# Kernel optimization log

Measured on AMD Instinct MI355X. Metric: run time of the kernel, lower is better.

Reference implementation:

```python
import jax, jax.numpy as jnp
import numpy as np

D_MODEL = 1024
NUM_HEADS = 16
HEAD_DIM = D_MODEL // NUM_HEADS


def setup_inputs() -> dict:
    key = jax.random.key(0)
    ks = jax.random.split(key, 10)
    s = 1.0 / np.sqrt(D_MODEL)
    return {
        "x": jax.random.normal(ks[0], (2, 2048, D_MODEL), dtype=jnp.float32),
        "Wq": jax.random.normal(ks[1], (D_MODEL, D_MODEL), dtype=jnp.float32) * s,
        "bq": jnp.zeros((D_MODEL,), jnp.float32),
        "Wk": jax.random.normal(ks[2], (D_MODEL, D_MODEL), dtype=jnp.float32) * s,
        "bk": jnp.zeros((D_MODEL,), jnp.float32),
        "Wv": jax.random.normal(ks[3], (D_MODEL, D_MODEL), dtype=jnp.float32) * s,
        "bv": jnp.zeros((D_MODEL,), jnp.float32),
        "Wo": jax.random.normal(ks[4], (D_MODEL, D_MODEL), dtype=jnp.float32) * s,
        "bo": jnp.zeros((D_MODEL,), jnp.float32),
        "rotary": jax.random.normal(ks[5], (1, 1, HEAD_DIM), dtype=jnp.float32) * 0.02,
    }


def reference(x, Wq, bq, Wk, bk, Wv, bv, Wo, bo, rotary):
    B, S, _ = x.shape
    H, Dh = NUM_HEADS, HEAD_DIM
    q = (x @ Wq + bq).reshape(B, S, H, Dh)
    k = (x @ Wk + bk).reshape(B, S, H, Dh)
    v = (x @ Wv + bv).reshape(B, S, H, Dh)
    # additive learned bias broadcast over (B, S, H) -> rotary has shape (1,1,Dh)
    q_rot = q + rotary[:, :, None, :]  # (B,S,H,Dh)
    scale = 1.0 / jnp.sqrt(jnp.asarray(Dh, jnp.float32))
    attn = jnp.einsum('bqhd,bkhd->bhqk', q_rot, k) * scale
    attn = jax.nn.softmax(attn, axis=-1)  # dropout is identity in eval / p=0
    out = jnp.einsum('bhqk,bkhd->bqhd', attn, v).reshape(B, S, H * Dh)
    return out @ Wo + bo
```

## Files before the change

### kernel.cpp

```cpp
#include <hip/hip_runtime.h>
#include <hip/hip_bf16.h>
#include <hip/hip_fp16.h>
#include <cstdint>

typedef _Float16 f16;
typedef _Float16 f16x4 __attribute__((ext_vector_type(4)));
typedef _Float16 f16x8 __attribute__((ext_vector_type(8)));
typedef __fp16 h16x2 __attribute__((ext_vector_type(2)));
typedef float f32x4 __attribute__((ext_vector_type(4)));

constexpr int D_MODEL = 1024;
constexpr int NH = 16;
constexpr int DH = 64;
constexpr int BATCH = 2;
constexpr int SEQ = 2048;
constexpr int NTOK = BATCH * SEQ;

static __device__ __forceinline__ void gld_lds16(const void* g, void* l) {
  __builtin_amdgcn_global_load_lds(
      (__attribute__((address_space(1))) void*)(g),
      (__attribute__((address_space(3))) void*)(l), 16, 0, 0);
}

static __device__ __forceinline__ f16x4 pack4(float a, float b, float c, float d) {
  h16x2 lo = __builtin_amdgcn_cvt_pkrtz(a, b);
  h16x2 hi = __builtin_amdgcn_cvt_pkrtz(c, d);
  struct { h16x2 x, y; } pr{lo, hi};
  return __builtin_bit_cast(f16x4, pr);
}


__global__ void cvt_x(const float* __restrict__ x, f16* __restrict__ xh) {
  int i = blockIdx.x * blockDim.x + threadIdx.x;
  const float4* p = reinterpret_cast<const float4*>(x) + (size_t)i * 2;
  float4 a = p[0], b = p[1];
  f16x8 o;
  o[0] = (f16)a.x; o[1] = (f16)a.y; o[2] = (f16)a.z; o[3] = (f16)a.w;
  o[4] = (f16)b.x; o[5] = (f16)b.y; o[6] = (f16)b.z; o[7] = (f16)b.w;
  *reinterpret_cast<f16x8*>(xh + (size_t)i * 8) = o;
}

__global__ void cvt_w(const float* __restrict__ Wq, const float* __restrict__ Wk,
                      const float* __restrict__ Wv, const float* __restrict__ Wo,
                      f16* __restrict__ Wqkvt, f16* __restrict__ Wot) {
  __shared__ float tile[32][33];
  int z = blockIdx.z;
  const float* src = (z == 0) ? Wq : (z == 1) ? Wk : (z == 2) ? Wv : Wo;
  f16* dst = (z < 3) ? (Wqkvt + (size_t)z * D_MODEL * D_MODEL) : Wot;
  int n0 = blockIdx.x * 32, k0 = blockIdx.y * 32;
  int tx = threadIdx.x & 31, ty = threadIdx.x >> 5;
#pragma unroll
  for (int j = 0; j < 32; j += 8)
    tile[ty + j][tx] = src[(size_t)(k0 + ty + j) * D_MODEL + n0 + tx];
  __syncthreads();
#pragma unroll
  for (int j = 0; j < 32; j += 8)
    dst[(size_t)(n0 + ty + j) * D_MODEL + k0 + tx] = (f16)tile[tx][ty + j];
}

__global__ void transpose_v(const f16* __restrict__ V, f16* __restrict__ Vt) {
  __shared__ __align__(16) f16 t[64 * 64];
  const int bh = blockIdx.y, s0 = blockIdx.x * 64;
  const f16* src = V + ((size_t)bh * SEQ + s0) * DH;
  f16* dst = Vt + (size_t)bh * DH * SEQ + s0;
  const int i = threadIdx.x;
#pragma unroll
  for (int p = 0; p < 2; ++p) {
    int seg = p * 256 + i;
    int s = seg >> 3, d0 = (seg & 7) * 8;
    f16x8 v = *reinterpret_cast<const f16x8*>(src + (size_t)s * DH + d0);
#pragma unroll
    for (int j = 0; j < 8; ++j) {
      int d = d0 + j;
      int swz = ((s >> 3) ^ (d & 7) ^ ((d >> 3) & 7)) & 7;
      t[d * 64 + swz * 8 + (s & 7)] = v[j];
    }
  }
  __syncthreads();
#pragma unroll
  for (int p = 0; p < 2; ++p) {
    int seg = p * 256 + i;
    int d = seg >> 3, c0 = (seg & 7) * 8;
    int swz = ((c0 >> 3) ^ (d & 7) ^ ((d >> 3) & 7)) & 7;
    f16x8 v = *reinterpret_cast<const f16x8*>(&t[d * 64 + swz * 8]);
    *reinterpret_cast<f16x8*>(dst + (size_t)d * SEQ + c0) = v;
  }
}


template <int MODE>
__global__ __launch_bounds__(256, 2) void gemm128(
    const f16* __restrict__ A, const f16* __restrict__ Bt,
    const float* __restrict__ b0, const float* __restrict__ b1,
    const float* __restrict__ b2, const float* __restrict__ rot,
    f16* __restrict__ oq, f16* __restrict__ ok, f16* __restrict__ ov,
    float* __restrict__ oOut) {
  constexpr int K = 1024;
  constexpr int BK = 64;
  __shared__ __align__(16) f16 As[128 * BK];
  __shared__ __align__(16) f16 Bs[128 * BK];
  const int tid = threadIdx.x;
  const int w = tid >> 6, lane = tid & 63;
  const int tot = gridDim.x;
  const int flat = blockIdx.x;
  const int nf = (flat & 7) * (tot >> 3) + (flat >> 3);
  const int bx = nf >> 5, by = nf & 31;
  const int m0 = by * 128, n0 = bx * 128;
  const int wr = (w >> 1) * 64, wc = (w & 1) * 64;
  const int lr = lane & 15, lg = lane >> 4;

  f32x4 acc[4][4] = {};

  auto stage = [&](int kt) {
#pragma unroll
    for (int i = 0; i < 4; ++i) {
      int seg = (w * 4 + i) * 64 + lane;
      int row = seg >> 3, col = (seg & 7) * 8;
      gld_lds16(A + (size_t)(m0 + row) * K + kt + col, &As[seg * 8]);
      gld_lds16(Bt + (size_t)(n0 + row) * K + kt + col, &Bs[seg * 8]);
    }
  };

  stage(0);
#pragma unroll 1
  for (int kt = 0; kt < K; kt += BK) {
    __syncthreads();
#pragma unroll
    for (int kk = 0; kk < BK; kk += 32) {
      f16x8 af[4], bf[4];
#pragma unroll
      for (int mi = 0; mi < 4; ++mi)
        af[mi] = *reinterpret_cast<const f16x8*>(&As[(wr + mi * 16 + lr) * BK + kk + lg * 8]);
#pragma unroll
      for (int ni = 0; ni < 4; ++ni)
        bf[ni] = *reinterpret_cast<const f16x8*>(&Bs[(wc + ni * 16 + lr) * BK + kk + lg * 8]);
#pragma unroll
      for (int mi = 0; mi < 4; ++mi)
#pragma unroll
        for (int ni = 0; ni < 4; ++ni)
          acc[mi][ni] = __builtin_amdgcn_mfma_f32_16x16x32_f16(af[mi], bf[ni], acc[mi][ni], 0, 0, 0);
    }
    __syncthreads();
    if (kt + BK < K) stage(kt + BK);
  }

#pragma unroll
  for (int mi = 0; mi < 4; ++mi) {
    int rowb = m0 + wr + mi * 16 + lg * 4;
#pragma unroll
    for (int ni = 0; ni < 4; ++ni) {
      int col = n0 + wc + ni * 16 + lr;
#pragma unroll
      for (int r = 0; r < 4; ++r) {
        float val = acc[mi][ni][r];
        int m = rowb + r;
        if (MODE == 0) {
          int which = col >> 10, rest = col & 1023;
          int hh = rest >> 6, d = rest & 63;
          int bb = m >> 11, ss = m & 2047;
          size_t dst = ((size_t)(bb * NH + hh) * SEQ + ss) * DH + d;
          if (which == 0) {
            oq[dst] = (f16)((val + b0[rest] + rot[d]) * (0.125f * 1.4426950408889634f));
          } else if (which == 1) {
            ok[dst] = (f16)(val + b1[rest]);
          } else {
            ov[dst] = (f16)(val + b2[rest]);
          }
        } else {
          oOut[(size_t)m * D_MODEL + col] = val + b0[col];
        }
      }
    }
  }
}

__global__ __launch_bounds__(256, 4) void attn(
    const f16* __restrict__ Qg, const f16* __restrict__ Kg,
    const f16* __restrict__ Vtg, f16* __restrict__ Og) {
  __shared__ __align__(16) f16 Ks[2][64 * 64];
  __shared__ __align__(16) f16 Vs[2][64 * 64];
  __shared__ __align__(16) f16 Ps[4][16 * 64];
  const int tid = threadIdx.x, w = tid >> 6, lane = tid & 63;
  const int lr = lane & 15, lg = lane >> 4;
  const int b = blockIdx.x;
  const int xcd = b & 7, j = b >> 3;
  const int bh = xcd * 4 + (j & 3);
  const int qb = j >> 2;
  const int q0 = qb * 64 + w * 16;
  const f16* Qb = Qg + (size_t)bh * SEQ * DH;
  const f16* Kb = Kg + (size_t)bh * SEQ * DH;
  const f16* Vtb = Vtg + (size_t)bh * DH * SEQ;

  f16x8 aq[2];
#pragma unroll
  for (int ks = 0; ks < 2; ++ks)
    aq[ks] = *reinterpret_cast<const f16x8*>(Qb + (size_t)(q0 + lr) * DH + ks * 32 + lg * 8);

  float mi = -1e30f, li = 0.f;
  f32x4 accO[4] = {};

  auto stage = [&](int buf, int t) {
#pragma unroll
    for (int i = 0; i < 2; ++i) {
      int seg = (w * 2 + i) * 64 + lane;
      int row = seg >> 3, c = seg & 7;
      int sc8 = (c ^ (row & 7)) * 8;
      gld_lds16(Kb + (size_t)(t + row) * DH + sc8, &Ks[buf][seg * 8]);
      gld_lds16(Vtb + (size_t)row * SEQ + t + sc8, &Vs[buf][seg * 8]);
    }
  };

  stage(0, 0);
  int cur = 0;
#pragma unroll 1
  for (int t = 0; t < SEQ; t += 64) {
    __syncthreads();
    if (t + 64 < SEQ) stage(cur ^ 1, t + 64);

    f32x4 sc[4];
#pragma unroll
    for (int kt2 = 0; kt2 < 4; ++kt2) {
      f32x4 z = {};
#pragma unroll
      for (int ks = 0; ks < 2; ++ks) {
        f16x8 kf = *reinterpret_cast<const f16x8*>(
            &Ks[cur][(kt2 * 16 + lr) * 64 + ((ks * 4 + lg) ^ (lr & 7)) * 8]);
        z = __builtin_amdgcn_mfma_f32_16x16x32_f16(kf, aq[ks], z, 0, 0, 0);
      }
      sc[kt2] = z;
    }

    float pm = sc[0][0];
#pragma unroll
    for (int kt2 = 0; kt2 < 4; ++kt2)
#pragma unroll
      for (int r = 0; r < 4; ++r) pm = fmaxf(pm, sc[kt2][r]);
    pm = fmaxf(pm, __shfl_xor(pm, 16));
    pm = fmaxf(pm, __shfl_xor(pm, 32));
    if (!__all(pm <= mi + 8.f)) {
      float nm = fmaxf(mi, pm);
      float sc8 = __builtin_amdgcn_exp2f(mi - nm);
      mi = nm;
      li *= sc8;
#pragma unroll
      for (int ct = 0; ct < 4; ++ct)
#pragma unroll
        for (int r = 0; r < 4; ++r) accO[ct][r] *= sc8;
    }
    float rs = 0.f;
#pragma unroll
    for (int kt2 = 0; kt2 < 4; ++kt2)
#pragma unroll
      for (int r = 0; r < 4; ++r) {
        float p = __builtin_amdgcn_exp2f(sc[kt2][r] - mi);
        sc[kt2][r] = p;
        rs += p;
      }
    rs += __shfl_xor(rs, 16);
    rs += __shfl_xor(rs, 32);
    li += rs;
#pragma unroll
    for (int kt2 = 0; kt2 < 4; ++kt2) {
      f16x4 pk = pack4(sc[kt2][0], sc[kt2][1], sc[kt2][2], sc[kt2][3]);
      int addr = lr * 64 + (((kt2 * 2 + (lg >> 1)) ^ (lr & 7)) * 8) + (lg & 1) * 4;
      *reinterpret_cast<f16x4*>(&Ps[w][addr]) = pk;
    }

#pragma unroll
    for (int ks = 0; ks < 2; ++ks) {
      f16x8 ap = *reinterpret_cast<const f16x8*>(
          &Ps[w][lr * 64 + ((ks * 4 + lg) ^ (lr & 7)) * 8]);
#pragma unroll
      for (int ct = 0; ct < 4; ++ct) {
        f16x8 bv = *reinterpret_cast<const f16x8*>(
            &Vs[cur][(ct * 16 + lr) * 64 + ((ks * 4 + lg) ^ (lr & 7)) * 8]);
        accO[ct] = __builtin_amdgcn_mfma_f32_16x16x32_f16(bv, ap, accO[ct], 0, 0, 0);
      }
    }
    cur ^= 1;
  }

  const int bb = bh >> 4, hh = bh & 15;
  float inv = 1.f / li;
  f16* dst = Og + (size_t)(bb * SEQ + q0 + lr) * D_MODEL + hh * DH;
#pragma unroll
  for (int ct = 0; ct < 4; ++ct) {
    f16x4 pk = pack4(accO[ct][0] * inv, accO[ct][1] * inv,
                     accO[ct][2] * inv, accO[ct][3] * inv);
    *reinterpret_cast<f16x4*>(dst + ct * 16 + lg * 4) = pk;
  }
}


extern "C" void kernel_launch(void* const* d_in, const int* in_sizes, int n_in,
                              void* d_out, int out_size, void* d_ws, size_t ws_size,
                              hipStream_t stream) {
  const float* x  = (const float*)d_in[0];
  const float* Wq = (const float*)d_in[1];
  const float* bq = (const float*)d_in[2];
  const float* Wk = (const float*)d_in[3];
  const float* bk = (const float*)d_in[4];
  const float* Wv = (const float*)d_in[5];
  const float* bv = (const float*)d_in[6];
  const float* Wo = (const float*)d_in[7];
  const float* bo = (const float*)d_in[8];
  const float* rot = (const float*)d_in[9];

  char* wsb = (char*)d_ws;
  f16* Xh    = (f16*)(wsb);
  f16* Wqkvt = (f16*)(wsb + ((size_t)8 << 20));
  f16* Wot   = (f16*)(wsb + ((size_t)14 << 20));
  f16* Qa    = (f16*)(wsb + ((size_t)16 << 20));
  f16* Ka    = (f16*)(wsb + ((size_t)24 << 20));
  f16* Va    = (f16*)(wsb + ((size_t)32 << 20));
  f16* Oa    = (f16*)(wsb + ((size_t)40 << 20));
  f16* Vta   = (f16*)(wsb + ((size_t)48 << 20));

  cvt_x<<<dim3(NTOK * D_MODEL / (8 * 256)), dim3(256), 0, stream>>>(x, Xh);
  cvt_w<<<dim3(32, 32, 4), dim3(256), 0, stream>>>(Wq, Wk, Wv, Wo, Wqkvt, Wot);

  gemm128<0><<<dim3(3 * D_MODEL / 128 * (NTOK / 128)), dim3(256), 0, stream>>>(
      Xh, Wqkvt, bq, bk, bv, rot, Qa, Ka, Va, nullptr);

  transpose_v<<<dim3(SEQ / 64, BATCH * NH), dim3(256), 0, stream>>>(Va, Vta);

  attn<<<dim3((SEQ / 64) * BATCH * NH), dim3(256), 0, stream>>>(Qa, Ka, Vta, Oa);

  gemm128<1><<<dim3(D_MODEL / 128 * (NTOK / 128)), dim3(256), 0, stream>>>(
      Oa, Wot, bo, nullptr, nullptr, nullptr, nullptr, nullptr, nullptr,
      (float*)d_out);
}
```

Measured before the change: 222.3 us.

## Double-buffer GEMM LDS tiles and process two query fragments per attention wave

```diff
diff --git a/kernel.cpp b/kernel.cpp
--- a/kernel.cpp
+++ b/kernel.cpp
@@ -97,8 +97,8 @@
     float* __restrict__ oOut) {
   constexpr int K = 1024;
   constexpr int BK = 64;
-  __shared__ __align__(16) f16 As[128 * BK];
-  __shared__ __align__(16) f16 Bs[128 * BK];
+  __shared__ __align__(16) f16 As[2][128 * BK];
+  __shared__ __align__(16) f16 Bs[2][128 * BK];
   const int tid = threadIdx.x;
   const int w = tid >> 6, lane = tid & 63;
   const int tot = gridDim.x;
@@ -111,37 +111,38 @@
 
   f32x4 acc[4][4] = {};
 
-  auto stage = [&](int kt) {
+  auto stage = [&](int buf, int kt) {
 #pragma unroll
     for (int i = 0; i < 4; ++i) {
       int seg = (w * 4 + i) * 64 + lane;
       int row = seg >> 3, col = (seg & 7) * 8;
-      gld_lds16(A + (size_t)(m0 + row) * K + kt + col, &As[seg * 8]);
-      gld_lds16(Bt + (size_t)(n0 + row) * K + kt + col, &Bs[seg * 8]);
+      gld_lds16(A + (size_t)(m0 + row) * K + kt + col, &As[buf][seg * 8]);
+      gld_lds16(Bt + (size_t)(n0 + row) * K + kt + col, &Bs[buf][seg * 8]);
     }
   };
 
-  stage(0);
+  stage(0, 0);
+  int cur = 0;
 #pragma unroll 1
   for (int kt = 0; kt < K; kt += BK) {
     __syncthreads();
+    if (kt + BK < K) stage(cur ^ 1, kt + BK);
 #pragma unroll
     for (int kk = 0; kk < BK; kk += 32) {
       f16x8 af[4], bf[4];
 #pragma unroll
       for (int mi = 0; mi < 4; ++mi)
-        af[mi] = *reinterpret_cast<const f16x8*>(&As[(wr + mi * 16 + lr) * BK + kk + lg * 8]);
+        af[mi] = *reinterpret_cast<const f16x8*>(&As[cur][(wr + mi * 16 + lr) * BK + kk + lg * 8]);
 #pragma unroll
       for (int ni = 0; ni < 4; ++ni)
-        bf[ni] = *reinterpret_cast<const f16x8*>(&Bs[(wc + ni * 16 + lr) * BK + kk + lg * 8]);
+        bf[ni] = *reinterpret_cast<const f16x8*>(&Bs[cur][(wc + ni * 16 + lr) * BK + kk + lg * 8]);
 #pragma unroll
       for (int mi = 0; mi < 4; ++mi)
 #pragma unroll
         for (int ni = 0; ni < 4; ++ni)
           acc[mi][ni] = __builtin_amdgcn_mfma_f32_16x16x32_f16(af[mi], bf[ni], acc[mi][ni], 0, 0, 0);
     }
-    __syncthreads();
-    if (kt + BK < K) stage(kt + BK);
+    cur ^= 1;
   }
 
 #pragma unroll
@@ -174,30 +175,33 @@
   }
 }
 
-__global__ __launch_bounds__(256, 4) void attn(
+__global__ __launch_bounds__(256, 2) void attn(
     const f16* __restrict__ Qg, const f16* __restrict__ Kg,
     const f16* __restrict__ Vtg, f16* __restrict__ Og) {
   __shared__ __align__(16) f16 Ks[2][64 * 64];
   __shared__ __align__(16) f16 Vs[2][64 * 64];
-  __shared__ __align__(16) f16 Ps[4][16 * 64];
+  __shared__ __align__(16) f16 Ps[4][32 * 64];
   const int tid = threadIdx.x, w = tid >> 6, lane = tid & 63;
   const int lr = lane & 15, lg = lane >> 4;
   const int b = blockIdx.x;
   const int xcd = b & 7, j = b >> 3;
   const int bh = xcd * 4 + (j & 3);
   const int qb = j >> 2;
-  const int q0 = qb * 64 + w * 16;
+  const int q0 = qb * 128 + w * 32;
   const f16* Qb = Qg + (size_t)bh * SEQ * DH;
   const f16* Kb = Kg + (size_t)bh * SEQ * DH;
   const f16* Vtb = Vtg + (size_t)bh * DH * SEQ;
 
-  f16x8 aq[2];
-#pragma unroll
-  for (int ks = 0; ks < 2; ++ks)
-    aq[ks] = *reinterpret_cast<const f16x8*>(Qb + (size_t)(q0 + lr) * DH + ks * 32 + lg * 8);
-
-  float mi = -1e30f, li = 0.f;
-  f32x4 accO[4] = {};
+  f16x8 aq[2][2];
+#pragma unroll
+  for (int qf = 0; qf < 2; ++qf)
+#pragma unroll
+    for (int ks = 0; ks < 2; ++ks)
+      aq[qf][ks] = *reinterpret_cast<const f16x8*>(
+          Qb + (size_t)(q0 + qf * 16 + lr) * DH + ks * 32 + lg * 8);
+
+  float mi[2] = {-1e30f, -1e30f}, li[2] = {0.f, 0.f};
+  f32x4 accO[2][4] = {};
 
   auto stage = [&](int buf, int t) {
 #pragma unroll
@@ -217,77 +221,89 @@
     __syncthreads();
     if (t + 64 < SEQ) stage(cur ^ 1, t + 64);
 
-    f32x4 sc[4];
+    f32x4 sc[2][4];
 #pragma unroll
     for (int kt2 = 0; kt2 < 4; ++kt2) {
-      f32x4 z = {};
+      f32x4 z0 = {}, z1 = {};
 #pragma unroll
       for (int ks = 0; ks < 2; ++ks) {
         f16x8 kf = *reinterpret_cast<const f16x8*>(
             &Ks[cur][(kt2 * 16 + lr) * 64 + ((ks * 4 + lg) ^ (lr & 7)) * 8]);
-        z = __builtin_amdgcn_mfma_f32_16x16x32_f16(kf, aq[ks], z, 0, 0, 0);
-      }
-      sc[kt2] = z;
-    }
-
-    float pm = sc[0][0];
-#pragma unroll
-    for (int kt2 = 0; kt2 < 4; ++kt2)
-#pragma unroll
-      for (int r = 0; r < 4; ++r) pm = fmaxf(pm, sc[kt2][r]);
-    pm = fmaxf(pm, __shfl_xor(pm, 16));
-    pm = fmaxf(pm, __shfl_xor(pm, 32));
-    if (!__all(pm <= mi + 8.f)) {
-      float nm = fmaxf(mi, pm);
-      float sc8 = __builtin_amdgcn_exp2f(mi - nm);
-      mi = nm;
-      li *= sc8;
-#pragma unroll
-      for (int ct = 0; ct < 4; ++ct)
-#pragma unroll
-        for (int r = 0; r < 4; ++r) accO[ct][r] *= sc8;
-    }
-    float rs = 0.f;
-#pragma unroll
-    for (int kt2 = 0; kt2 < 4; ++kt2)
-#pragma unroll
-      for (int r = 0; r < 4; ++r) {
-        float p = __builtin_amdgcn_exp2f(sc[kt2][r] - mi);
-        sc[kt2][r] = p;
-        rs += p;
-      }
-    rs += __shfl_xor(rs, 16);
-    rs += __shfl_xor(rs, 32);
-    li += rs;
-#pragma unroll
-    for (int kt2 = 0; kt2 < 4; ++kt2) {
-      f16x4 pk = pack4(sc[kt2][0], sc[kt2][1], sc[kt2][2], sc[kt2][3]);
-      int addr = lr * 64 + (((kt2 * 2 + (lg >> 1)) ^ (lr & 7)) * 8) + (lg & 1) * 4;
-      *reinterpret_cast<f16x4*>(&Ps[w][addr]) = pk;
+        z0 = __builtin_amdgcn_mfma_f32_16x16x32_f16(kf, aq[0][ks], z0, 0, 0, 0);
+        z1 = __builtin_amdgcn_mfma_f32_16x16x32_f16(kf, aq[1][ks], z1, 0, 0, 0);
+      }
+      sc[0][kt2] = z0;
+      sc[1][kt2] = z1;
+    }
+
+#pragma unroll
+    for (int qf = 0; qf < 2; ++qf) {
+      float pm = sc[qf][0][0];
+#pragma unroll
+      for (int kt2 = 0; kt2 < 4; ++kt2)
+#pragma unroll
+        for (int r = 0; r < 4; ++r) pm = fmaxf(pm, sc[qf][kt2][r]);
+      pm = fmaxf(pm, __shfl_xor(pm, 16));
+      pm = fmaxf(pm, __shfl_xor(pm, 32));
+      if (!__all(pm <= mi[qf] + 8.f)) {
+        float nm = fmaxf(mi[qf], pm);
+        float s8 = __builtin_amdgcn_exp2f(mi[qf] - nm);
+        mi[qf] = nm;
+        li[qf] *= s8;
+#pragma unroll
+        for (int ct = 0; ct < 4; ++ct)
+#pragma unroll
+          for (int r = 0; r < 4; ++r) accO[qf][ct][r] *= s8;
+      }
+      float rs = 0.f;
+#pragma unroll
+      for (int kt2 = 0; kt2 < 4; ++kt2)
+#pragma unroll
+        for (int r = 0; r < 4; ++r) {
+          float p = __builtin_amdgcn_exp2f(sc[qf][kt2][r] - mi[qf]);
+          sc[qf][kt2][r] = p;
+          rs += p;
+        }
+      rs += __shfl_xor(rs, 16);
+      rs += __shfl_xor(rs, 32);
+      li[qf] += rs;
+#pragma unroll
+      for (int kt2 = 0; kt2 < 4; ++kt2) {
+        f16x4 pk = pack4(sc[qf][kt2][0], sc[qf][kt2][1], sc[qf][kt2][2], sc[qf][kt2][3]);
+        int addr = (qf * 16 + lr) * 64 +
+                   (((kt2 * 2 + (lg >> 1)) ^ (lr & 7)) * 8) + (lg & 1) * 4;
+        *reinterpret_cast<f16x4*>(&Ps[w][addr]) = pk;
+      }
     }
 
 #pragma unroll
     for (int ks = 0; ks < 2; ++ks) {
-      f16x8 ap = *reinterpret_cast<const f16x8*>(
+      f16x8 ap0 = *reinterpret_cast<const f16x8*>(
           &Ps[w][lr * 64 + ((ks * 4 + lg) ^ (lr & 7)) * 8]);
+      f16x8 ap1 = *reinterpret_cast<const f16x8*>(
+          &Ps[w][(16 + lr) * 64 + ((ks * 4 + lg) ^ (lr & 7)) * 8]);
 #pragma unroll
       for (int ct = 0; ct < 4; ++ct) {
         f16x8 bv = *reinterpret_cast<const f16x8*>(
             &Vs[cur][(ct * 16 + lr) * 64 + ((ks * 4 + lg) ^ (lr & 7)) * 8]);
-        accO[ct] = __builtin_amdgcn_mfma_f32_16x16x32_f16(bv, ap, accO[ct], 0, 0, 0);
+        accO[0][ct] = __builtin_amdgcn_mfma_f32_16x16x32_f16(bv, ap0, accO[0][ct], 0, 0, 0);
+        accO[1][ct] = __builtin_amdgcn_mfma_f32_16x16x32_f16(bv, ap1, accO[1][ct], 0, 0, 0);
       }
     }
     cur ^= 1;
   }
 
   const int bb = bh >> 4, hh = bh & 15;
-  float inv = 1.f / li;
-  f16* dst = Og + (size_t)(bb * SEQ + q0 + lr) * D_MODEL + hh * DH;
-#pragma unroll
-  for (int ct = 0; ct < 4; ++ct) {
-    f16x4 pk = pack4(accO[ct][0] * inv, accO[ct][1] * inv,
-                     accO[ct][2] * inv, accO[ct][3] * inv);
-    *reinterpret_cast<f16x4*>(dst + ct * 16 + lg * 4) = pk;
+#pragma unroll
+  for (int qf = 0; qf < 2; ++qf) {
+    float inv = 1.f / li[qf];
+    f16* dst = Og + (size_t)(bb * SEQ + q0 + qf * 16 + lr) * D_MODEL + hh * DH;
+#pragma unroll
+    for (int ct = 0; ct < 4; ++ct) {
+      f16x4 pk = pack4(accO[qf][ct][0] * inv, accO[qf][ct][1] * inv,
+                       accO[qf][ct][2] * inv, accO[qf][ct][3] * inv);
+      *reinterpret_cast<f16x4*>(dst + ct * 16 + lg * 4) = pk;
+    }
   }
 }
 
@@ -324,7 +340,7 @@
 
   transpose_v<<<dim3(SEQ / 64, BATCH * NH), dim3(256), 0, stream>>>(Va, Vta);
 
-  attn<<<dim3((SEQ / 64) * BATCH * NH), dim3(256), 0, stream>>>(Qa, Ka, Vta, Oa);
+  attn<<<dim3((SEQ / 128) * BATCH * NH), dim3(256), 0, stream>>>(Qa, Ka, Vta, Oa);
 
   gemm128<1><<<dim3(D_MODEL / 128 * (NTOK / 128)), dim3(256), 0, stream>>>(
       Oa, Wot, bo, nullptr, nullptr, nullptr, nullptr, nullptr, nullptr,
```

New measurement: 245.1 us. 1.1x slower.
